# Optimization experiments

Measured on AMD Instinct MI355X. Metric: run time of the kernel, lower is better.

Reference implementation:

```python
import jax, jax.numpy as jnp
import numpy as np

C = 192
DCT = 7
EPS = 1e-5
LOW_X = [0,0,1,1,0,2,2,1,2,0,3,4,0,1,3,0,1,2,3,4,5,0,1,2,3,4,5,6,1,2,3,4]
LOW_Y = [0,1,0,1,2,0,1,2,2,3,0,0,4,3,1,5,4,3,2,1,0,6,5,4,3,2,1,0,6,5,4,3]


def _dct_basis():
    # basis[i, tx, ty] = bf(tx, ux_i, DCT) * bf(ty, vy_i, DCT)
    t = jnp.arange(DCT, dtype=jnp.float32)
    fx = jnp.array(LOW_X, dtype=jnp.float32)  # mapper scale = dct_h//7 = 1
    fy = jnp.array(LOW_Y, dtype=jnp.float32)
    def bf(freq):
        r = jnp.cos(jnp.pi * freq[:, None] * (t[None, :] + 0.5) / DCT) / jnp.sqrt(jnp.float32(DCT))
        return jnp.where(freq[:, None] == 0, r, r * jnp.sqrt(jnp.float32(2.0)))
    bx, by = bf(fx), bf(fy)  # [32, 7] each
    return bx[:, :, None] * by[:, None, :]  # [32, 7, 7]


def reference(x, wg1, bn2_g, bn2_b, bn2_m, bn2_v, wg2, bg2, beta, w1d, b1d, bn1_g, bn1_b, bn1_m, bn1_v):
    n, c, h, w = x.shape
    # gate: 1x1 conv -> BN2d (eval) -> ReLU -> global avg pool -> 1x1 conv
    g = jnp.einsum('nchw,oc->nohw', x, wg1)
    g = (g - bn2_m[None, :, None, None]) * (bn2_g / jnp.sqrt(bn2_v + EPS))[None, :, None, None] + bn2_b[None, :, None, None]
    g = jax.nn.relu(g).mean(axis=(2, 3))          # [n, 32]
    xg = g @ wg2.T + bg2                           # [n, 32]
    xg = jax.nn.relu(jnp.tanh(xg)) + beta          # gate_ac + beta
    # data-dependent channel partition from batch element 0 (torch uses .item() -> detached)
    xg0 = jax.lax.stop_gradient(xg[0])
    s = xg0.sum()
    p_mid = jnp.round(xg0[:31] / s * c)            # param[1..31]
    param = jnp.concatenate([jnp.zeros(1, jnp.float32), p_mid,
                             (jnp.float32(c) - p_mid.sum())[None]])  # [33]
    # build DCT filter: slice param[i]:param[i+1] gets basis i, later i overwrites
    ch = jnp.arange(c, dtype=jnp.float32)
    basis = _dct_basis()                           # [32, 7, 7]
    filt = jnp.zeros((c, DCT, DCT), jnp.float32)
    for i in range(32):
        m = (ch >= param[i]) & (ch < param[i + 1])
        filt = jnp.where(m[:, None, None], basis[i], filt)
    xp = x.reshape(n, c, DCT, h // DCT, DCT, w // DCT).mean(axis=(3, 5))
    y = jnp.sum(xp * filt[None], axis=(2, 3))      # [n, c] weighted spatial pooling
    # Conv1d(c, c, k=3, pad=1) on length-1 sequence: only center tap w1d[:, :, 1]
    y = y @ w1d[:, :, 1].T + b1d
    y = (y - bn1_m) * (bn1_g / jnp.sqrt(bn1_v + EPS)) + bn1_b
    y = jax.nn.relu(y)
    return x * y[:, :, None, None] + x


def setup_inputs() -> dict:
    key = jax.random.key(0)
    ks = jax.random.split(key, 16)
    n, h, w = 64, 56, 56
    return {
        'x':     jax.random.normal(ks[0], (n, C, h, w), jnp.float32),
        'wg1':   jax.random.normal(ks[1], (32, C), jnp.float32) * (2.0 / C) ** 0.5,
        'bn2_g': jax.random.uniform(ks[2], (32,), jnp.float32, 0.8, 1.2),
        'bn2_b': jax.random.normal(ks[3], (32,), jnp.float32) * 0.1,
        'bn2_m': jax.random.normal(ks[4], (32,), jnp.float32) * 0.1,
        'bn2_v': jax.random.uniform(ks[5], (32,), jnp.float32, 0.5, 1.5),
        'wg2':   jax.random.normal(ks[6], (32, 32), jnp.float32) * (2.0 / 32) ** 0.5,
        'bg2':   jax.random.normal(ks[7], (32,), jnp.float32) * 0.1,
        'beta':  jax.random.uniform(ks[8], (1,), jnp.float32, 0.05, 0.25),
        'w1d':   jax.random.normal(ks[9], (C, C, 3), jnp.float32) * (2.0 / (3 * C)) ** 0.5,
        'b1d':   jax.random.normal(ks[10], (C,), jnp.float32) * 0.1,
        'bn1_g': jax.random.uniform(ks[11], (C,), jnp.float32, 0.8, 1.2),
        'bn1_b': jax.random.normal(ks[12], (C,), jnp.float32) * 0.1,
        'bn1_m': jax.random.normal(ks[13], (C,), jnp.float32) * 0.1,
        'bn1_v': jax.random.uniform(ks[14], (C,), jnp.float32, 0.5, 1.5),
    }
```

## Files before the change

kernel.cpp:

```cpp
#include <hip/hip_runtime.h>
#include <hip/hip_bf16.h>
#include <math.h>

#define CCH 192
#define EPS 1e-5f

typedef float vfloat4 __attribute__((ext_vector_type(4)));

__device__ __constant__ int d_LOWX[32] = {0,0,1,1,0,2,2,1,2,0,3,4,0,1,3,0,1,2,3,4,5,0,1,2,3,4,5,6,1,2,3,4};
__device__ __constant__ int d_LOWY[32] = {0,1,0,1,2,0,1,2,2,3,0,0,4,3,1,5,4,3,2,1,0,6,5,4,3,2,1,0,6,5,4,3};

__global__ __launch_bounds__(256) void fused_pre_kernel(
    const float* __restrict__ x, const float* __restrict__ w1d,
    const float* __restrict__ wg1,
    const float* __restrict__ bn2_g, const float* __restrict__ bn2_b,
    const float* __restrict__ bn2_m, const float* __restrict__ bn2_v,
    float* __restrict__ xp, float* __restrict__ wt, float* __restrict__ partial) {
  __shared__ float smem[4 * 32 * 64];
  const int b = blockIdx.x;
  const int t = threadIdx.x;
  if (b < 3072) {
    const int n = b / 48, g = b % 48;
    const int wv = t >> 6, lane = t & 63;
    const int c0 = g * 4, c = c0 + wv;
    if (t < 196) smem[t] = 0.f;
    __syncthreads();
    const vfloat4* xv = (const vfloat4*)(x + (size_t)(n * CCH + c) * 3136);
#pragma unroll
    for (int it = 0; it < 13; ++it) {
      int f = it * 64 + lane;
      if (f < 784) {
        vfloat4 v = xv[f];
        int hh = f / 14;
        int wq = f - hh * 14;
        int cell = (hh >> 3) * 7 + (wq >> 1);
        atomicAdd(&smem[wv * 49 + cell], v.x + v.y + v.z + v.w);
      }
    }
    __syncthreads();
    if (t < 196) xp[((size_t)n * CCH + c0) * 49 + t] = smem[t] * (1.f / 64.f);
  } else if (b < 3216) {
    const int i = (b - 3072) * 256 + t;
    const int c = i / CCH, k = i - c * CCH;
    wt[k * CCH + c] = w1d[c * (CCH * 3) + 3 * k + 1];
  } else {
    const int h = b - 3216;
    const int cq = t >> 6;
    const int w  = t & 63;
    float acc[32];
#pragma unroll
    for (int o = 0; o < 32; ++o) acc[o] = 0.f;
    const float* xrow = x + h * 56;
    for (int c = cq * 48; c < cq * 48 + 48; ++c) {
      float xvv = (w < 56) ? xrow[c * 3136 + w] : 0.f;
#pragma unroll
      for (int o = 0; o < 32; ++o) acc[o] += xvv * wg1[o * 192 + c];
    }
#pragma unroll
    for (int o = 0; o < 32; ++o) smem[(cq * 32 + o) * 64 + w] = acc[o];
    __syncthreads();
    for (int e = t; e < 32 * 56; e += 256) {
      int o = e / 56, ww = e % 56;
      float v = smem[(0 * 32 + o) * 64 + ww] + smem[(1 * 32 + o) * 64 + ww] +
                smem[(2 * 32 + o) * 64 + ww] + smem[(3 * 32 + o) * 64 + ww];
      float sc = bn2_g[o] * rsqrtf(bn2_v[o] + EPS);
      v = v * sc + (bn2_b[o] - bn2_m[o] * sc);
      smem[o * 64 + ww] = fmaxf(v, 0.f);
    }
    __syncthreads();
    if (t < 32) {
      float s = 0.f;
      for (int ww = 0; ww < 56; ++ww) s += smem[t * 64 + ww];
      partial[h * 32 + t] = s;
    }
  }
}

__global__ __launch_bounds__(256) void mid_kernel(
    const float* __restrict__ partial, const float* __restrict__ wg2,
    const float* __restrict__ bg2, const float* __restrict__ beta,
    float* __restrict__ filt) {
  __shared__ float gm[32];
  __shared__ float xg[32];
  __shared__ float param[33];
  __shared__ float Btab[7][7];
  const int t = threadIdx.x;
  if (t < 32) {
    float s = 0.f;
    for (int hh = 0; hh < 56; ++hh) s += partial[hh * 32 + t];
    gm[t] = s * (1.f / 3136.f);
  }
  if (t < 49) {
    int f = t / 7, tt = t % 7;
    float r = cosf(3.14159265358979323846f * (float)f * ((float)tt + 0.5f) / 7.f) * rsqrtf(7.f);
    Btab[f][tt] = (f == 0) ? r : r * sqrtf(2.f);
  }
  __syncthreads();
  if (t < 32) {
    float a = bg2[t];
    for (int k = 0; k < 32; ++k) a += gm[k] * wg2[t * 32 + k];
    xg[t] = fmaxf(tanhf(a), 0.f) + beta[0];
  }
  __syncthreads();
  if (t == 0) {
    float s = 0.f;
    for (int k = 0; k < 32; ++k) s += xg[k];
    float psum = 0.f;
    param[0] = 0.f;
    for (int i = 0; i < 31; ++i) {
      float p = rintf(xg[i] / s * (float)CCH);
      param[i + 1] = p;
      psum += p;
    }
    param[32] = (float)CCH - psum;
  }
  __syncthreads();
  for (int c = t; c < CCH; c += 256) {
    int bi = -1;
    float cf = (float)c;
    for (int i = 0; i < 32; ++i)
      if (cf >= param[i] && cf < param[i + 1]) bi = i;
    int fx = (bi >= 0) ? d_LOWX[bi] : 0;
    int fy = (bi >= 0) ? d_LOWY[bi] : 0;
    for (int cell = 0; cell < 49; ++cell) {
      int a = cell / 7, bb = cell % 7;
      float v = (bi >= 0) ? Btab[fx][a] * Btab[fy][bb] : 0.f;
      filt[c * 49 + cell] = v;
    }
  }
}

__global__ __launch_bounds__(256) void gemv_scale_kernel(
    const float* __restrict__ xp, const float* __restrict__ filt,
    const float* __restrict__ wt, const float* __restrict__ b1d,
    const float* __restrict__ bn1_g, const float* __restrict__ bn1_b,
    const float* __restrict__ bn1_m, const float* __restrict__ bn1_v,
    float* __restrict__ scale) {
  __shared__ float yl[CCH];
  const int n = blockIdx.x, t = threadIdx.x;
  if (t < CCH) {
    const float* xc = xp + ((size_t)n * CCH + t) * 49;
    const float* fc = filt + t * 49;
    float s = 0.f;
#pragma unroll
    for (int cell = 0; cell < 49; ++cell) s += xc[cell] * fc[cell];
    yl[t] = s;
  }
  __syncthreads();
  if (t < CCH) {
    float acc = b1d[t];
    for (int k = 0; k < CCH; ++k) acc += yl[k] * wt[k * CCH + t];
    float sc = bn1_g[t] * rsqrtf(bn1_v[t] + EPS);
    float v = (acc - bn1_m[t]) * sc + bn1_b[t];
    scale[n * CCH + t] = 1.f + fmaxf(v, 0.f);
  }
}

__global__ __launch_bounds__(256) void apply_kernel(
    const float* __restrict__ x, const float* __restrict__ scale,
    float* __restrict__ out) {
  const int f = blockIdx.x * 256 + threadIdx.x;
  const int nc = f / 784;
  const float s = scale[nc];
  vfloat4 v = __builtin_nontemporal_load(((const vfloat4*)x) + f);
  v *= s;
  __builtin_nontemporal_store(v, ((vfloat4*)out) + f);
}

extern "C" void kernel_launch(void* const* d_in, const int* in_sizes, int n_in,
                              void* d_out, int out_size, void* d_ws, size_t ws_size,
                              hipStream_t stream) {
  const float* x     = (const float*)d_in[0];
  const float* wg1   = (const float*)d_in[1];
  const float* bn2_g = (const float*)d_in[2];
  const float* bn2_b = (const float*)d_in[3];
  const float* bn2_m = (const float*)d_in[4];
  const float* bn2_v = (const float*)d_in[5];
  const float* wg2   = (const float*)d_in[6];
  const float* bg2   = (const float*)d_in[7];
  const float* beta  = (const float*)d_in[8];
  const float* w1d   = (const float*)d_in[9];
  const float* b1d   = (const float*)d_in[10];
  const float* bn1_g = (const float*)d_in[11];
  const float* bn1_b = (const float*)d_in[12];
  const float* bn1_m = (const float*)d_in[13];
  const float* bn1_v = (const float*)d_in[14];
  float* out = (float*)d_out;

  float* ws      = (float*)d_ws;
  float* partial = ws;
  float* filt    = partial + 1792;
  float* wt      = filt + 9408;
  float* xp      = wt + 36864;
  float* scale   = xp + 602112;

  fused_pre_kernel<<<3272, 256, 0, stream>>>(x, w1d, wg1, bn2_g, bn2_b, bn2_m, bn2_v,
                                             xp, wt, partial);
  mid_kernel<<<1, 256, 0, stream>>>(partial, wg2, bg2, beta, filt);
  gemv_scale_kernel<<<64, 256, 0, stream>>>(xp, filt, wt, b1d, bn1_g, bn1_b, bn1_m, bn1_v, scale);
  apply_kernel<<<37632, 256, 0, stream>>>(x, scale, out);
}
```

Measured before the change: 359.0 us.

## Replace LDS atomics with shuffle reductions in pooling and gate-conv paths

The adaptive-pool path now has each lane load two float4s per 8-row band and reduces them with wavefront shuffles, replacing shared-memory atomics. The gate-conv blocks now assign 8 output channels per wave over all 192 input channels and reduce across width with xor shuffles, which removes the large shared buffer and two block barriers. The apply kernel switches the input load from nontemporal to a normal load, and the 1D-conv GEMV loop gets an unroll pragma. Each gate-conv wave now reads all 192 input channels instead of 48, so x-row loads per block grow fourfold in exchange for fewer partial sums.

```diff
diff --git a/kernel.cpp b/kernel.cpp
--- a/kernel.cpp
+++ b/kernel.cpp
@@ -16,62 +16,60 @@
     const float* __restrict__ bn2_g, const float* __restrict__ bn2_b,
     const float* __restrict__ bn2_m, const float* __restrict__ bn2_v,
     float* __restrict__ xp, float* __restrict__ wt, float* __restrict__ partial) {
-  __shared__ float smem[4 * 32 * 64];
+  __shared__ float smem[4 * 49];
   const int b = blockIdx.x;
   const int t = threadIdx.x;
   if (b < 3072) {
-    const int n = b / 48, g = b % 48;
-    const int wv = t >> 6, lane = t & 63;
-    const int c0 = g * 4, c = c0 + wv;
-    if (t < 196) smem[t] = 0.f;
-    __syncthreads();
+    const int n = b / 48, c0 = (b % 48) * 4;
+    const int wv = t >> 6, l = t & 63;
+    const int c = c0 + wv;
+    const bool act = l < 56;
+    const int lidx = act ? l : 0;
     const vfloat4* xv = (const vfloat4*)(x + (size_t)(n * CCH + c) * 3136);
-#pragma unroll
-    for (int it = 0; it < 13; ++it) {
-      int f = it * 64 + lane;
-      if (f < 784) {
-        vfloat4 v = xv[f];
-        int hh = f / 14;
-        int wq = f - hh * 14;
-        int cell = (hh >> 3) * 7 + (wq >> 1);
-        atomicAdd(&smem[wv * 49 + cell], v.x + v.y + v.z + v.w);
-      }
+    float acc[7];
+#pragma unroll
+    for (int g = 0; g < 7; ++g) {
+      vfloat4 v0 = xv[g * 112 + lidx];
+      vfloat4 v1 = xv[g * 112 + 56 + lidx];
+      float s = (v0.x + v0.y + v0.z + v0.w) + (v1.x + v1.y + v1.z + v1.w);
+      acc[g] = act ? s : 0.f;
+    }
+#pragma unroll
+    for (int g = 0; g < 7; ++g) {
+      float a = acc[g] + __shfl_xor(acc[g], 1);
+      a += __shfl(a, l + 28);
+      a += __shfl(a, l + 14);
+      if (act && l < 14 && (l & 1) == 0)
+        smem[wv * 49 + g * 7 + (l >> 1)] = a;
     }
     __syncthreads();
     if (t < 196) xp[((size_t)n * CCH + c0) * 49 + t] = smem[t] * (1.f / 64.f);
   } else if (b < 3216) {
     const int i = (b - 3072) * 256 + t;
-    const int c = i / CCH, k = i - c * CCH;
-    wt[k * CCH + c] = w1d[c * (CCH * 3) + 3 * k + 1];
+    const int cc = i / CCH, k = i - cc * CCH;
+    wt[k * CCH + cc] = w1d[cc * (CCH * 3) + 3 * k + 1];
   } else {
     const int h = b - 3216;
-    const int cq = t >> 6;
-    const int w  = t & 63;
-    float acc[32];
-#pragma unroll
-    for (int o = 0; o < 32; ++o) acc[o] = 0.f;
+    const int wv = t >> 6, w = t & 63;
+    float acc[8];
+#pragma unroll
+    for (int o = 0; o < 8; ++o) acc[o] = 0.f;
     const float* xrow = x + h * 56;
-    for (int c = cq * 48; c < cq * 48 + 48; ++c) {
-      float xvv = (w < 56) ? xrow[c * 3136 + w] : 0.f;
-#pragma unroll
-      for (int o = 0; o < 32; ++o) acc[o] += xvv * wg1[o * 192 + c];
-    }
-#pragma unroll
-    for (int o = 0; o < 32; ++o) smem[(cq * 32 + o) * 64 + w] = acc[o];
-    __syncthreads();
-    for (int e = t; e < 32 * 56; e += 256) {
-      int o = e / 56, ww = e % 56;
-      float v = smem[(0 * 32 + o) * 64 + ww] + smem[(1 * 32 + o) * 64 + ww] +
-                smem[(2 * 32 + o) * 64 + ww] + smem[(3 * 32 + o) * 64 + ww];
-      float sc = bn2_g[o] * rsqrtf(bn2_v[o] + EPS);
-      v = v * sc + (bn2_b[o] - bn2_m[o] * sc);
-      smem[o * 64 + ww] = fmaxf(v, 0.f);
-    }
-    __syncthreads();
-    if (t < 32) {
-      float s = 0.f;
-      for (int ww = 0; ww < 56; ++ww) s += smem[t * 64 + ww];
-      partial[h * 32 + t] = s;
+    for (int cc = 0; cc < CCH; ++cc) {
+      float xvv = (w < 56) ? xrow[cc * 3136 + w] : 0.f;
+#pragma unroll
+      for (int o = 0; o < 8; ++o)
+        acc[o] += xvv * wg1[(wv * 8 + o) * CCH + cc];
+    }
+#pragma unroll
+    for (int o = 0; o < 8; ++o) {
+      const int oo = wv * 8 + o;
+      float sc = bn2_g[oo] * rsqrtf(bn2_v[oo] + EPS);
+      float v = acc[o] * sc + (bn2_b[oo] - bn2_m[oo] * sc);
+      v = (w < 56) ? fmaxf(v, 0.f) : 0.f;
+#pragma unroll
+      for (int s = 1; s < 64; s <<= 1) v += __shfl_xor(v, s);
+      if (w == 0) partial[h * 32 + oo] = v;
     }
   }
 }
@@ -149,6 +147,7 @@
   __syncthreads();
   if (t < CCH) {
     float acc = b1d[t];
+#pragma unroll 4
     for (int k = 0; k < CCH; ++k) acc += yl[k] * wt[k * CCH + t];
     float sc = bn1_g[t] * rsqrtf(bn1_v[t] + EPS);
     float v = (acc - bn1_m[t]) * sc + bn1_b[t];
@@ -162,7 +161,7 @@
   const int f = blockIdx.x * 256 + threadIdx.x;
   const int nc = f / 784;
   const float s = scale[nc];
-  vfloat4 v = __builtin_nontemporal_load(((const vfloat4*)x) + f);
+  vfloat4 v = ((const vfloat4*)x)[f];
   v *= s;
   __builtin_nontemporal_store(v, ((vfloat4*)out) + f);
 }
```

Result: no change. 358.9 us (-0.0%).
